# Performance work log

Hardware: AMD Instinct MI355X
Metric: run time of the kernel (lower is better)

Reference implementation:

```python
import jax, jax.numpy as jnp
import numpy as np

D_MODEL = 4096
NUM_EXPERTS = 64
TOP_K = 2


def setup_inputs() -> dict:
    key = jax.random.key(0)
    k1, k2 = jax.random.split(key)
    hidden_states = jax.random.normal(k1, (4, 4096, D_MODEL), dtype=jnp.float32)
    # nn.Linear(d_model, num_experts, bias=False) weight: [num_experts, d_model]
    W = jax.random.normal(k2, (NUM_EXPERTS, D_MODEL), dtype=jnp.float32) * (1.0 / np.sqrt(D_MODEL))
    return {"hidden_states": hidden_states, "W": W}


def reference(hidden_states, W):
    # router_logits: [B, S, E]
    router_logits = jnp.einsum("bsd,ed->bse", hidden_states, W)
    # top-k over experts (torch.topk returns values sorted descending; lax.top_k matches)
    top_k_logits, top_k_indices = jax.lax.top_k(router_logits, TOP_K)
    routing_weights = jax.nn.softmax(top_k_logits, axis=-1)
    return routing_weights, top_k_indices
```

## Files before the change

### kernel.cpp

```cpp
#include <hip/hip_runtime.h>
#include <stdint.h>

#define D_MODEL 4096
#define N_EXP   64
#define N_TOK   16384
#define MTILE   32
#define KC      128
#define NCHUNK  (D_MODEL / KC)

typedef float  f32x4  __attribute__((ext_vector_type(4)));
typedef short  bf16x8 __attribute__((ext_vector_type(8)));

__device__ __forceinline__ void cvt8(float4 v0, float4 v1, bf16x8& hi, bf16x8& lo) {
  float f[8] = {v0.x, v0.y, v0.z, v0.w, v1.x, v1.y, v1.z, v1.w};
#pragma unroll
  for (int i = 0; i < 8; ++i) {
    unsigned u  = __builtin_bit_cast(unsigned, f[i]);
    unsigned r  = u + 0x7FFFu + ((u >> 16) & 1u);
    unsigned hb = r & 0xFFFF0000u;
    float    res = f[i] - __builtin_bit_cast(float, hb);
    hi[i] = (short)(hb >> 16);
    lo[i] = (short)(__builtin_bit_cast(unsigned, res) >> 16);
  }
}

__global__ __launch_bounds__(256) void prep_w_kernel(
    const float* __restrict__ W, short* __restrict__ Wh, short* __restrict__ Wl)
{
  const int t  = blockIdx.x * 256 + threadIdx.x;
  const int e  = t & 63;
  const int kg = t >> 6;
  const float* src = W + (size_t)e * D_MODEL + kg * 8;
  float4 a = *(const float4*)src;
  float4 b = *(const float4*)(src + 4);
  bf16x8 hi, lo;
  cvt8(a, b, hi, lo);
  *(bf16x8*)(Wh + ((size_t)kg * 64 + e) * 8) = hi;
  *(bf16x8*)(Wl + ((size_t)kg * 64 + e) * 8) = lo;
}

__global__ __launch_bounds__(256) void SimpleMoERouter_54219667144993_kernel(
    const float* __restrict__ X, const short* __restrict__ Wh,
    const short* __restrict__ Wl, float* __restrict__ outw, float* __restrict__ outi)
{
  __shared__ uint4 sX[2][MTILE * KC / 4];
  __shared__ float sRed[MTILE][N_EXP + 1];

  const int tid  = threadIdx.x;
  const int lane = tid & 63;
  const int wv   = tid >> 6;
  const int tok0 = blockIdx.x * MTILE;
  const int r16  = lane & 15;
  const int kq   = lane >> 4;
  const int mh   = wv & 1;
  const int nh   = wv >> 1;
  const int arow = mh * 16 + r16;
  const int rs   = arow & 15;

  const float* xbase = X + (size_t)tok0 * D_MODEL;

  auto STAGE = [&](int c, int b) {
#pragma unroll
    for (int q = 0; q < 4; ++q) {
      const int G   = q * 256 + tid;
      const int row = G >> 5;
      const int col = G & 31;
      const int sc  = col ^ (row & 15);
      const float* src = xbase + (size_t)row * D_MODEL + (size_t)c * KC + sc * 4;
      __builtin_amdgcn_global_load_lds(
          (const __attribute__((address_space(1))) void*)src,
          (__attribute__((address_space(3))) void*)&sX[b][q * 256 + wv * 64],
          16, 0, 0);
    }
  };

  f32x4 acc[2] = {{0.f,0.f,0.f,0.f},{0.f,0.f,0.f,0.f}};

  STAGE(0, 0);
  __syncthreads();

  int b = 0;
  for (int c = 0; c < NCHUNK; ++c) {
    if (c + 1 < NCHUNK) STAGE(c + 1, b ^ 1);
#pragma unroll
    for (int s = 0; s < 4; ++s) {
      const int cg = s * 8 + kq * 2;
      uint4 g0 = sX[b][arow * 32 + (cg ^ rs)];
      uint4 g1 = sX[b][arow * 32 + ((cg + 1) ^ rs)];
      bf16x8 ah, al;
      cvt8(__builtin_bit_cast(float4, g0), __builtin_bit_cast(float4, g1), ah, al);
      const size_t wg = ((size_t)c * 16 + s * 4 + kq) * 64;
#pragma unroll
      for (int j = 0; j < 2; ++j) {
        const size_t wi = (wg + (size_t)(nh * 2 + j) * 16 + r16) * 8;
        bf16x8 bh = *(const bf16x8*)(Wh + wi);
        bf16x8 bl = *(const bf16x8*)(Wl + wi);
        acc[j] = __builtin_amdgcn_mfma_f32_16x16x32_bf16(ah, bh, acc[j], 0, 0, 0);
        acc[j] = __builtin_amdgcn_mfma_f32_16x16x32_bf16(ah, bl, acc[j], 0, 0, 0);
        acc[j] = __builtin_amdgcn_mfma_f32_16x16x32_bf16(al, bh, acc[j], 0, 0, 0);
      }
    }
    __syncthreads();
    b ^= 1;
  }

#pragma unroll
  for (int j = 0; j < 2; ++j)
#pragma unroll
    for (int r = 0; r < 4; ++r)
      sRed[mh * 16 + kq * 4 + r][nh * 32 + j * 16 + r16] = acc[j][r];
  __syncthreads();

  if (tid < MTILE) {
    float best = -3.4e38f, sec = -3.4e38f;
    int bi = 0, si = 0;
#pragma unroll 8
    for (int e = 0; e < N_EXP; ++e) {
      const float v = sRed[tid][e];
      const bool b1 = v > best;
      const bool b2 = v > sec;
      sec  = b1 ? best : (b2 ? v : sec);
      si   = b1 ? bi   : (b2 ? e : si);
      best = b1 ? v : best;
      bi   = b1 ? e : bi;
    }
    const float ed  = expf(sec - best);
    const float inv = 1.0f / (1.0f + ed);
    const int gt = tok0 + tid;
    outw[2 * gt]     = inv;
    outw[2 * gt + 1] = ed * inv;
    outi[2 * gt]     = (float)bi;
    outi[2 * gt + 1] = (float)si;
  }
}

extern "C" void kernel_launch(void* const* d_in, const int* in_sizes, int n_in,
                              void* d_out, int out_size, void* d_ws, size_t ws_size,
                              hipStream_t stream) {
  const float* X = (const float*)d_in[0];
  const float* W = (const float*)d_in[1];
  float* outw = (float*)d_out;
  float* outi = (float*)d_out + (size_t)N_TOK * 2;
  short* Wh = (short*)d_ws;
  short* Wl = (short*)d_ws + (size_t)N_EXP * D_MODEL;

  hipLaunchKernelGGL(prep_w_kernel, dim3(128), dim3(256), 0, stream, W, Wh, Wl);
  hipLaunchKernelGGL(SimpleMoERouter_54219667144993_kernel,
                     dim3(N_TOK / MTILE), dim3(256), 0, stream,
                     X, Wh, Wl, outw, outi);
}
```

Baseline: 420.4 us.

## Software-pipeline W fragment loads into registers one chunk ahead

```diff
diff --git a/kernel.cpp b/kernel.cpp
--- a/kernel.cpp
+++ b/kernel.cpp
@@ -39,7 +39,31 @@
   *(bf16x8*)(Wl + ((size_t)kg * 64 + e) * 8) = lo;
 }
 
-__global__ __launch_bounds__(256) void SimpleMoERouter_54219667144993_kernel(
+#define LOADW(dst, c) do {                                              \
+  _Pragma("unroll")                                                     \
+  for (int t_ = 0; t_ < 8; ++t_) {                                      \
+    const size_t wg_ = ((size_t)(c) * 16 + (t_ >> 1) * 4 + kq) * 64;    \
+    const size_t wi_ = (wg_ + (size_t)(nh * 2 + (t_ & 1)) * 16 + r16) * 8; \
+    dst[2 * t_]     = *(const bf16x8*)(Wh + wi_);                       \
+    dst[2 * t_ + 1] = *(const bf16x8*)(Wl + wi_);                       \
+  } } while (0)
+
+#define COMPUTE(bb, w) do {                                             \
+  _Pragma("unroll")                                                     \
+  for (int s_ = 0; s_ < 4; ++s_) {                                      \
+    const int cg_ = s_ * 8 + kq * 2;                                    \
+    uint4 g0_ = sX[bb][arow * 32 + (cg_ ^ rs)];                         \
+    uint4 g1_ = sX[bb][arow * 32 + ((cg_ + 1) ^ rs)];                   \
+    bf16x8 ah_, al_;                                                    \
+    cvt8(__builtin_bit_cast(float4, g0_), __builtin_bit_cast(float4, g1_), ah_, al_); \
+    _Pragma("unroll")                                                   \
+    for (int j_ = 0; j_ < 2; ++j_) {                                    \
+      acc[j_] = __builtin_amdgcn_mfma_f32_16x16x32_bf16(ah_, w[2*(s_*2+j_)],   acc[j_], 0, 0, 0); \
+      acc[j_] = __builtin_amdgcn_mfma_f32_16x16x32_bf16(ah_, w[2*(s_*2+j_)+1], acc[j_], 0, 0, 0); \
+      acc[j_] = __builtin_amdgcn_mfma_f32_16x16x32_bf16(al_, w[2*(s_*2+j_)],   acc[j_], 0, 0, 0); \
+    } } } while (0)
+
+__global__ __launch_bounds__(256, 2) void SimpleMoERouter_54219667144993_kernel(
     const float* __restrict__ X, const short* __restrict__ Wh,
     const short* __restrict__ Wl, float* __restrict__ outw, float* __restrict__ outi)
 {
@@ -75,33 +99,23 @@
   };
 
   f32x4 acc[2] = {{0.f,0.f,0.f,0.f},{0.f,0.f,0.f,0.f}};
+  bf16x8 wA[16], wB[16];
 
+  LOADW(wA, 0);
   STAGE(0, 0);
   __syncthreads();
 
-  int b = 0;
-  for (int c = 0; c < NCHUNK; ++c) {
-    if (c + 1 < NCHUNK) STAGE(c + 1, b ^ 1);
-#pragma unroll
-    for (int s = 0; s < 4; ++s) {
-      const int cg = s * 8 + kq * 2;
-      uint4 g0 = sX[b][arow * 32 + (cg ^ rs)];
-      uint4 g1 = sX[b][arow * 32 + ((cg + 1) ^ rs)];
-      bf16x8 ah, al;
-      cvt8(__builtin_bit_cast(float4, g0), __builtin_bit_cast(float4, g1), ah, al);
-      const size_t wg = ((size_t)c * 16 + s * 4 + kq) * 64;
-#pragma unroll
-      for (int j = 0; j < 2; ++j) {
-        const size_t wi = (wg + (size_t)(nh * 2 + j) * 16 + r16) * 8;
-        bf16x8 bh = *(const bf16x8*)(Wh + wi);
-        bf16x8 bl = *(const bf16x8*)(Wl + wi);
-        acc[j] = __builtin_amdgcn_mfma_f32_16x16x32_bf16(ah, bh, acc[j], 0, 0, 0);
-        acc[j] = __builtin_amdgcn_mfma_f32_16x16x32_bf16(ah, bl, acc[j], 0, 0, 0);
-        acc[j] = __builtin_amdgcn_mfma_f32_16x16x32_bf16(al, bh, acc[j], 0, 0, 0);
-      }
+  for (int c = 0; c < NCHUNK; c += 2) {
+    STAGE(c + 1, 1);
+    LOADW(wB, c + 1);
+    COMPUTE(0, wA);
+    __syncthreads();
+    if (c + 2 < NCHUNK) {
+      STAGE(c + 2, 0);
+      LOADW(wA, c + 2);
     }
+    COMPUTE(1, wB);
     __syncthreads();
-    b ^= 1;
   }
 
 #pragma unroll
```

Measured after the change: 364.7 us. 1.15x faster.
